# Optimization experiments

Measured on AMD Instinct MI355X. Metric: run time of the kernel, lower is better.

Reference implementation:

```python
import jax, jax.numpy as jnp
import numpy as np

N_NODES = 100000


def sage_conv(x, src, dst, W_l, W_r, b):
    """PyG-style SAGEConv with mean aggregation:
    out = mean_{j in N(i)} x_j @ W_l + b + x_i @ W_r
    Messages flow edge_index[0] (src) -> edge_index[1] (dst).
    """
    n = x.shape[0]
    msgs = x[src]  # [E, F] gather
    agg = jax.ops.segment_sum(msgs, dst, num_segments=n)  # [N, F]
    cnt = jax.ops.segment_sum(jnp.ones((src.shape[0],), dtype=x.dtype), dst, num_segments=n)
    mean = agg / jnp.clip(cnt, 1.0)[:, None]
    return mean @ W_l + b + x @ W_r


def setup_inputs() -> dict:
    key = jax.random.key(0)
    ks = jax.random.split(key, 12)
    F_in, H, out_c = 128, 128, 1
    E, K = 3200000, 64

    def glorot(k, shape):
        fan_in, fan_out = shape[0], shape[1]
        lim = np.sqrt(6.0 / (fan_in + fan_out))
        return jax.random.uniform(k, shape, jnp.float32, -lim, lim)

    return {
        "x": jax.random.normal(ks[0], (N_NODES, F_in), jnp.float32),
        "edge_index": jax.random.randint(ks[1], (2, E), 0, N_NODES, jnp.int64),
        "curr_idx": 123,
        "dest_idx": 4567,
        "neighbor_indices": jax.random.randint(ks[2], (K,), 0, N_NODES, jnp.int64),
        # conv1 params
        "W1_l": glorot(ks[3], (F_in, H)),
        "W1_r": glorot(ks[4], (F_in, H)),
        "b1": jnp.zeros((H,), jnp.float32),
        # conv2 params
        "W2_l": glorot(ks[5], (H, H)),
        "W2_r": glorot(ks[6], (H, H)),
        "b2": jnp.zeros((H,), jnp.float32),
        # MLP head
        "Wlin1": glorot(ks[7], (3 * H, H)),
        "blin1": jnp.zeros((H,), jnp.float32),
        "Wlin2": glorot(ks[8], (H, out_c)),
        "blin2": jnp.zeros((out_c,), jnp.float32),
    }


def reference(x, edge_index, curr_idx, dest_idx, neighbor_indices,
              W1_l, W1_r, b1, W2_l, W2_r, b2, Wlin1, blin1, Wlin2, blin2):
    src, dst = edge_index[0], edge_index[1]
    h = jax.nn.relu(sage_conv(x, src, dst, W1_l, W1_r, b1))
    node_embs = sage_conv(h, src, dst, W2_l, W2_r, b2)  # [N, H]

    curr_emb = node_embs[curr_idx]  # [H]
    dest_emb = node_embs[dest_idx]  # [H]
    nbr_embs = node_embs[neighbor_indices]  # [K, H]
    K = nbr_embs.shape[0]
    # batched version of the per-neighbor concat + 2-layer MLP
    cat = jnp.concatenate([
        jnp.broadcast_to(curr_emb, (K, curr_emb.shape[0])),
        jnp.broadcast_to(dest_emb, (K, dest_emb.shape[0])),
        nbr_embs,
    ], axis=1)  # [K, 3H]
    hidden = jax.nn.relu(cat @ Wlin1 + blin1)  # [K, H]
    q_values = hidden @ Wlin2 + blin2  # [K, 1]
    return q_values
```

## Files before the change

### kernel.cpp

```cpp
#include <hip/hip_runtime.h>
#include <cstdint>

constexpr int F        = 128;
constexpr int U_CAP    = 8192;
constexpr int T_CAP    = 128;
constexpr int E2_CAP   = 131072;
constexpr int BKT      = 128;
constexpr int BM_WORDS = 3200;
constexpr int SBLK     = 256;
constexpr int EPT      = 64;
constexpr int EPBLK    = SBLK * EPT;
constexpr int LCAP     = 512;


__global__ void k_zero(int* p, int n) {
    int i = blockIdx.x * blockDim.x + threadIdx.x;
    int stride = gridDim.x * blockDim.x;
    for (; i < n; i += stride) p[i] = 0;
}

__global__ void k_build(const int* eidx, int E, int N,
                        const int* curr, const int* dest, const int* nbr, int K,
                        int* hdr, int* t_map, int* u_map,
                        unsigned* t_bm, unsigned* u_bm,
                        int* t_node, int* ent2comp, int* ulist) {
    __shared__ int s_e64, s_n64;
    int tid = threadIdx.x;
    if (tid == 0) { s_e64 = 1; s_n64 = 1; }
    __syncthreads();
    if (tid < 64 && eidx[2 * tid + 1] != 0) s_e64 = 0;
    if (tid < K / 2 && nbr[2 * tid + 1] != 0) s_n64 = 0;
    __syncthreads();
    int n64 = s_n64;
    if (tid == 0) { hdr[4] = s_e64; hdr[5] = s_n64; }

    int node = -1;
    if (tid < K + 2) {
        if (tid == 0)      node = curr[0];
        else if (tid == 1) node = dest[0];
        else               node = n64 ? nbr[2 * (tid - 2)] : nbr[tid - 2];
        if ((unsigned)node < (unsigned)N) {
            if (atomicCAS(&t_map[node], 0, -1) == 0) {
                int slot = atomicAdd(&hdr[0], 1);
                t_node[slot] = node;
                int uid = atomicAdd(&hdr[1], 1);
                ulist[uid] = node;
                atomicExch(&u_map[node], uid + 1);
                if (node < BM_WORDS * 32) {
                    atomicOr(&t_bm[node >> 5], 1u << (node & 31));
                    atomicOr(&u_bm[node >> 5], 1u << (node & 31));
                }
                atomicExch(&t_map[node], slot + 1);
            }
        }
    }
    __syncthreads();
    if (tid < K + 2) {
        int v = ((unsigned)node < (unsigned)N) ? atomicAdd(&t_map[node], 0) : 1;
        ent2comp[tid] = v - 1;
    }
}

static __device__ __forceinline__ int esrc(const int* eidx, int E, int e, int is64) {
    return is64 ? eidx[2 * (size_t)e] : eidx[e];
}
static __device__ __forceinline__ int edst(const int* eidx, int E, int e, int is64) {
    return is64 ? eidx[2 * ((size_t)E + e)] : eidx[(size_t)E + e];
}

__global__ void k_scan1(const int* __restrict__ eidx, int E, int N,
                        const int* __restrict__ t_map, int* u_map,
                        const unsigned* __restrict__ t_bm, unsigned* u_bm,
                        int* hdr, int2* edges2, int* ulist) {
    __shared__ int l_cnt, l_base;
    __shared__ int2 l_buf[LCAP];
    int tid = threadIdx.x;
    if (tid == 0) l_cnt = 0;
    __syncthreads();
    int is64 = hdr[4];
    int be = blockIdx.x * EPBLK;
    int dv[EPT];
    #pragma unroll
    for (int r = 0; r < EPT / 4; ++r) {
        int e0 = be + (r * SBLK + tid) * 4;
        if (!is64 && e0 + 3 < E) {
            int4 d4 = *reinterpret_cast<const int4*>(eidx + (size_t)E + e0);
            dv[r*4+0] = d4.x; dv[r*4+1] = d4.y; dv[r*4+2] = d4.z; dv[r*4+3] = d4.w;
        } else {
            for (int q = 0; q < 4; ++q)
                dv[r*4+q] = (e0 + q < E) ? edst(eidx, E, e0 + q, is64) : -1;
        }
    }
    unsigned long long m = 0;
    #pragma unroll
    for (int i = 0; i < EPT; ++i) {
        int d  = dv[i];
        int dc = ((unsigned)d < (unsigned)N) ? d : 0;
        unsigned w = t_bm[dc >> 5];
        if ((unsigned)d < (unsigned)N && ((w >> (d & 31)) & 1))
            m |= (1ull << i);
    }
    while (m) {
        int i = __ffsll(m) - 1; m &= m - 1;
        int d = dv[i];
        int tm = t_map[d];
        if (tm <= 0) continue;
        int r = i >> 2, q = i & 3;
        int e = be + (r * SBLK + tid) * 4 + q;
        int s = esrc(eidx, E, e, is64);
        if ((unsigned)s >= (unsigned)N) continue;
        int p = atomicAdd(&l_cnt, 1);
        if (p < LCAP) l_buf[p] = make_int2(s, tm - 1);
        else {
            int gp = atomicAdd(&hdr[2], 1);
            if (gp < E2_CAP) edges2[gp] = make_int2(s, tm - 1);
        }
        if (atomicCAS(&u_map[s], 0, -1) == 0) {
            int id = atomicAdd(&hdr[1], 1);
            if (id < U_CAP) ulist[id] = s;
            if (s < BM_WORDS * 32) atomicOr(&u_bm[s >> 5], 1u << (s & 31));
            __threadfence();
            atomicExch(&u_map[s], id + 1);
        }
    }
    __syncthreads();
    int c = min(l_cnt, LCAP);
    if (c > 0) {
        if (tid == 0) l_base = atomicAdd(&hdr[2], c);
        __syncthreads();
        for (int i = tid; i < c; i += SBLK) {
            int gp = l_base + i;
            if (gp < E2_CAP) edges2[gp] = l_buf[i];
        }
    }
}

__global__ void k_scanU(const int* __restrict__ eidx, int E, int N,
                        const int* __restrict__ u_map,
                        const unsigned* __restrict__ u_bm,
                        const int* __restrict__ hdr,
                        int* deg1, int* bucket) {
    int tid = threadIdx.x;
    int is64 = hdr[4];
    int be = blockIdx.x * EPBLK;
    int dv[EPT];
    #pragma unroll
    for (int r = 0; r < EPT / 4; ++r) {
        int e0 = be + (r * SBLK + tid) * 4;
        if (!is64 && e0 + 3 < E) {
            int4 d4 = *reinterpret_cast<const int4*>(eidx + (size_t)E + e0);
            dv[r*4+0] = d4.x; dv[r*4+1] = d4.y; dv[r*4+2] = d4.z; dv[r*4+3] = d4.w;
        } else {
            for (int q = 0; q < 4; ++q)
                dv[r*4+q] = (e0 + q < E) ? edst(eidx, E, e0 + q, is64) : -1;
        }
    }
    unsigned long long m = 0;
    #pragma unroll
    for (int i = 0; i < EPT; ++i) {
        int d  = dv[i];
        int dc = ((unsigned)d < (unsigned)N) ? d : 0;
        unsigned w = u_bm[dc >> 5];
        if ((unsigned)d < (unsigned)N && ((w >> (d & 31)) & 1))
            m |= (1ull << i);
    }
    while (m) {
        int i = __ffsll(m) - 1; m &= m - 1;
        int d = dv[i];
        int um = u_map[d];
        if (um <= 0 || um > U_CAP) continue;
        int r = i >> 2, q = i & 3;
        int e = be + (r * SBLK + tid) * 4 + q;
        int s = esrc(eidx, E, e, is64);
        if ((unsigned)s >= (unsigned)N) continue;
        int slot = um - 1;
        int pos = atomicAdd(&deg1[slot], 1);
        if (pos < BKT) bucket[(size_t)slot * BKT + pos] = s;
    }
}

__global__ void k_l1(const int* __restrict__ deg1, const int* __restrict__ bucket,
                     const int* __restrict__ hdr, const int* __restrict__ ulist, int N,
                     const float* __restrict__ x,
                     const float* __restrict__ W1l, const float* __restrict__ W1r,
                     const float* __restrict__ b1, float* __restrict__ h) {
    int nU = min(hdr[1], U_CAP);
    __shared__ int s_src[BKT];
    __shared__ float4 s_part[4][32];
    __shared__ float mean[F];
    __shared__ float xr[F];
    int j = threadIdx.x;
    int g = j >> 5, l = j & 31;
    for (int b = blockIdx.x; b < nU; b += gridDim.x) {
        int dg = deg1[b];
        int stored = min(dg, BKT);
        if (j < stored) s_src[j] = bucket[(size_t)b * BKT + j];
        int node = ulist[b];
        xr[j] = ((unsigned)node < (unsigned)N) ? x[(size_t)node * F + j] : 0.0f;
        __syncthreads();
        float4 a4 = make_float4(0.f, 0.f, 0.f, 0.f);
        #pragma unroll 4
        for (int i = g; i < stored; i += 4) {
            int s = s_src[i];
            if ((unsigned)s < (unsigned)N) {
                float4 v = reinterpret_cast<const float4*>(x + (size_t)s * F)[l];
                a4.x += v.x; a4.y += v.y; a4.z += v.z; a4.w += v.w;
            }
        }
        s_part[g][l] = a4;
        __syncthreads();
        float c = (dg < 1) ? 1.0f : (float)dg;
        int lp = j >> 2, cc = j & 3;
        float sum = 0.0f;
        #pragma unroll
        for (int gg = 0; gg < 4; ++gg) {
            float4 p = s_part[gg][lp];
            sum += (cc == 0) ? p.x : (cc == 1) ? p.y : (cc == 2) ? p.z : p.w;
        }
        mean[j] = sum / c;
        __syncthreads();
        float o = b1[j];
        #pragma unroll 4
        for (int k = 0; k < F; ++k) {
            o += mean[k] * W1l[k * F + j];
            o += xr[k]   * W1r[k * F + j];
        }
        h[(size_t)b * F + j] = (o > 0.0f) ? o : 0.0f;
        __syncthreads();
    }
}

__global__ void k_l2(const int* __restrict__ hdr, const int* __restrict__ t_node,
                     const int* __restrict__ u_map, int N,
                     const int2* __restrict__ edges2, const float* __restrict__ h,
                     const float* __restrict__ W2l, const float* __restrict__ W2r,
                     const float* __restrict__ b2, float* __restrict__ embT) {
    int nT = min(hdr[0], T_CAP);
    int b  = blockIdx.x;
    if (b >= nT) return;
    int nE2 = min(hdr[2], E2_CAP);
    __shared__ int s_ui[256];
    __shared__ int s_cnt;
    __shared__ float mean[F];
    __shared__ float hr[F];
    int j = threadIdx.x;
    if (j == 0) s_cnt = 0;
    __syncthreads();
    for (int i = j; i < nE2; i += 128) {
        int2 ed = edges2[i];
        if (ed.y == b) {
            int ui = ((unsigned)ed.x < (unsigned)N) ? (u_map[ed.x] - 1) : -1;
            if ((unsigned)ui < (unsigned)U_CAP) {
                int p = atomicAdd(&s_cnt, 1);
                if (p < 256) s_ui[p] = ui;
            }
        }
    }
    __syncthreads();
    int cnt = min(s_cnt, 256);
    float sum = 0.0f;
    #pragma unroll 4
    for (int i = 0; i < cnt; ++i) sum += h[(size_t)s_ui[i] * F + j];
    float c = (s_cnt < 1) ? 1.0f : (float)s_cnt;
    mean[j] = sum / c;
    int node = t_node[b];
    int ui = ((unsigned)node < (unsigned)N) ? (u_map[node] - 1) : -1;
    hr[j] = ((unsigned)ui < (unsigned)U_CAP) ? h[(size_t)ui * F + j] : 0.0f;
    __syncthreads();
    float acc = b2[j];
    #pragma unroll 4
    for (int k = 0; k < F; ++k) {
        acc += mean[k] * W2l[k * F + j];
        acc += hr[k]   * W2r[k * F + j];
    }
    embT[(size_t)b * F + j] = acc;
}

static __device__ __forceinline__ float clamp999(int v) {
    return (float)(v < 0 ? 0 : (v > 999 ? 999 : v));
}

__global__ void k_headf(const int* __restrict__ hdr, const int* __restrict__ ent2comp,
                        const float* __restrict__ embT,
                        const float* __restrict__ Wlin1, const float* __restrict__ blin1,
                        const float* __restrict__ Wlin2, const float* __restrict__ blin2,
                        float* __restrict__ out, int K) {
    __shared__ float s_cat[3 * F];
    __shared__ float s_part[4][F];
    __shared__ float red[F];
    int k = blockIdx.x;
    int tid = threadIdx.x;
    int g = tid >> 7, j = tid & (F - 1);
    int c0 = ent2comp[0] & (T_CAP - 1);
    int c1 = ent2comp[1] & (T_CAP - 1);
    int ck = ent2comp[2 + k] & (T_CAP - 1);
    if (tid < F)          s_cat[tid] = embT[(size_t)c0 * F + tid];
    else if (tid < 2 * F) s_cat[tid] = embT[(size_t)c1 * F + (tid - F)];
    else if (tid < 3 * F) s_cat[tid] = embT[(size_t)ck * F + (tid - 2 * F)];
    __syncthreads();
    float acc = 0.0f;
    #pragma unroll 4
    for (int i = g * 96; i < (g + 1) * 96; ++i)
        acc += s_cat[i] * Wlin1[i * F + j];
    s_part[g][j] = acc;
    __syncthreads();
    if (g == 0) {
        float hid = blin1[j] + s_part[0][j] + s_part[1][j] + s_part[2][j] + s_part[3][j];
        hid = (hid > 0.0f) ? hid : 0.0f;
        red[j] = hid * Wlin2[j];
    }
    __syncthreads();
    for (int s = 64; s > 0; s >>= 1) {
        if (tid < s) red[tid] += red[tid + s];
        __syncthreads();
    }
    if (tid == 0) {
        int nT = hdr[0], nU = hdr[1], nE2 = hdr[2];
        float D = 0.0f;
        if      (nT  < 1  || nT  > K + 2)  D = 1.0e6f + clamp999(nT) * 1e3f;
        else if (nU  < nT || nU  > U_CAP)  D = 2.0e6f + clamp999(nU / 10) * 1e3f;
        else if (nE2 < 1  || nE2 > E2_CAP) D = 3.0e6f + clamp999(nE2 / 10) * 1e3f;
        out[k] = red[0] + blin2[0] + D;
    }
}

extern "C" void kernel_launch(void* const* d_in, const int* in_sizes, int n_in,
                              void* d_out, int out_size, void* d_ws, size_t ws_size,
                              hipStream_t stream) {
    const float* x     = (const float*)d_in[0];
    const int*   eidx  = (const int*)d_in[1];
    const int*   curr  = (const int*)d_in[2];
    const int*   dest  = (const int*)d_in[3];
    const int*   nbr   = (const int*)d_in[4];
    const float* W1l   = (const float*)d_in[5];
    const float* W1r   = (const float*)d_in[6];
    const float* b1    = (const float*)d_in[7];
    const float* W2l   = (const float*)d_in[8];
    const float* W2r   = (const float*)d_in[9];
    const float* b2    = (const float*)d_in[10];
    const float* Wlin1 = (const float*)d_in[11];
    const float* blin1 = (const float*)d_in[12];
    const float* Wlin2 = (const float*)d_in[13];
    const float* blin2 = (const float*)d_in[14];
    float* out = (float*)d_out;

    const int N = in_sizes[0] / F;
    const int E = in_sizes[1] / 2;
    const int K = in_sizes[4];

    char*  ws  = (char*)d_ws;
    size_t off = 0;
    int*      hdr      = (int*)(ws + off);      off += 64;
    int*      t_map    = (int*)(ws + off);      off += (size_t)4 * N;
    int*      u_map    = (int*)(ws + off);      off += (size_t)4 * N;
    int*      t_node   = (int*)(ws + off);      off += (size_t)4 * T_CAP;
    int*      ent2comp = (int*)(ws + off);      off += (size_t)4 * 256;
    int*      ulist    = (int*)(ws + off);      off += (size_t)4 * U_CAP;
    unsigned* t_bm     = (unsigned*)(ws + off); off += (size_t)4 * BM_WORDS;
    unsigned* u_bm     = (unsigned*)(ws + off); off += (size_t)4 * BM_WORDS;
    int*      deg1     = (int*)(ws + off);      off += (size_t)4 * U_CAP;
    size_t zero_bytes = off;
    int*      bucket   = (int*)(ws + off);      off += (size_t)4 * U_CAP * BKT;
    int2*     edges2   = (int2*)(ws + off);     off += (size_t)8 * E2_CAP;
    float*    h        = (float*)(ws + off);    off += (size_t)4 * U_CAP * F;
    float*    embT     = (float*)(ws + off);    off += (size_t)4 * T_CAP * F;

    int zero_words = (int)(zero_bytes / 4);
    k_zero<<<1024, 256, 0, stream>>>((int*)d_ws, zero_words);

    k_build<<<1, 128, 0, stream>>>(eidx, E, N, curr, dest, nbr, K, hdr, t_map, u_map,
                                   t_bm, u_bm, t_node, ent2comp, ulist);

    int sg = (E + EPBLK - 1) / EPBLK;
    k_scan1<<<sg, SBLK, 0, stream>>>(eidx, E, N, t_map, u_map, t_bm, u_bm,
                                     hdr, edges2, ulist);
    k_scanU<<<sg, SBLK, 0, stream>>>(eidx, E, N, u_map, u_bm, hdr, deg1, bucket);
    k_l1<<<2048, 128, 0, stream>>>(deg1, bucket, hdr, ulist, N, x, W1l, W1r, b1, h);
    k_l2<<<T_CAP, 128, 0, stream>>>(hdr, t_node, u_map, N, edges2, h, W2l, W2r, b2, embT);
    k_headf<<<K, 512, 0, stream>>>(hdr, ent2comp, embT, Wlin1, blin1, Wlin2, blin2, out, K);
}
```

Baseline: 255.8 us.

## Reuse scanU buckets for layer-2 aggregation and vectorize int64 edge scans

The separate target-edge list built in the first scan is removed. Layer 2 now reads each target's in-neighbours from the per-node buckets that the second scan already fills, so the first scan only has to discover the 1-hop source set. Both scans process edges inline through a probe lambda instead of buffering 64 destinations per thread in registers. They read int64 edge indices with int4 vector loads, and edges per thread drop from 64 to 16. The cost is that layer 2 relies on bucket truncation at BKT, and the edge-list count check disappears from the diagnostics.

```diff
diff --git a/kernel.cpp b/kernel.cpp
--- a/kernel.cpp
+++ b/kernel.cpp
@@ -4,13 +4,11 @@
 constexpr int F        = 128;
 constexpr int U_CAP    = 8192;
 constexpr int T_CAP    = 128;
-constexpr int E2_CAP   = 131072;
 constexpr int BKT      = 128;
 constexpr int BM_WORDS = 3200;
 constexpr int SBLK     = 256;
-constexpr int EPT      = 64;
+constexpr int EPT      = 16;
 constexpr int EPBLK    = SBLK * EPT;
-constexpr int LCAP     = 512;
 
 
 __global__ void k_zero(int* p, int n) {
@@ -61,60 +59,20 @@
     }
 }
 
-static __device__ __forceinline__ int esrc(const int* eidx, int E, int e, int is64) {
-    return is64 ? eidx[2 * (size_t)e] : eidx[e];
-}
-static __device__ __forceinline__ int edst(const int* eidx, int E, int e, int is64) {
-    return is64 ? eidx[2 * ((size_t)E + e)] : eidx[(size_t)E + e];
-}
-
 __global__ void k_scan1(const int* __restrict__ eidx, int E, int N,
-                        const int* __restrict__ t_map, int* u_map,
-                        const unsigned* __restrict__ t_bm, unsigned* u_bm,
-                        int* hdr, int2* edges2, int* ulist) {
-    __shared__ int l_cnt, l_base;
-    __shared__ int2 l_buf[LCAP];
+                        int* __restrict__ u_map,
+                        const unsigned* __restrict__ t_bm,
+                        unsigned* __restrict__ u_bm,
+                        int* __restrict__ hdr, int* __restrict__ ulist) {
     int tid = threadIdx.x;
-    if (tid == 0) l_cnt = 0;
-    __syncthreads();
     int is64 = hdr[4];
-    int be = blockIdx.x * EPBLK;
-    int dv[EPT];
-    #pragma unroll
-    for (int r = 0; r < EPT / 4; ++r) {
-        int e0 = be + (r * SBLK + tid) * 4;
-        if (!is64 && e0 + 3 < E) {
-            int4 d4 = *reinterpret_cast<const int4*>(eidx + (size_t)E + e0);
-            dv[r*4+0] = d4.x; dv[r*4+1] = d4.y; dv[r*4+2] = d4.z; dv[r*4+3] = d4.w;
-        } else {
-            for (int q = 0; q < 4; ++q)
-                dv[r*4+q] = (e0 + q < E) ? edst(eidx, E, e0 + q, is64) : -1;
-        }
-    }
-    unsigned long long m = 0;
-    #pragma unroll
-    for (int i = 0; i < EPT; ++i) {
-        int d  = dv[i];
-        int dc = ((unsigned)d < (unsigned)N) ? d : 0;
-        unsigned w = t_bm[dc >> 5];
-        if ((unsigned)d < (unsigned)N && ((w >> (d & 31)) & 1))
-            m |= (1ull << i);
-    }
-    while (m) {
-        int i = __ffsll(m) - 1; m &= m - 1;
-        int d = dv[i];
-        int tm = t_map[d];
-        if (tm <= 0) continue;
-        int r = i >> 2, q = i & 3;
-        int e = be + (r * SBLK + tid) * 4 + q;
-        int s = esrc(eidx, E, e, is64);
-        if ((unsigned)s >= (unsigned)N) continue;
-        int p = atomicAdd(&l_cnt, 1);
-        if (p < LCAP) l_buf[p] = make_int2(s, tm - 1);
-        else {
-            int gp = atomicAdd(&hdr[2], 1);
-            if (gp < E2_CAP) edges2[gp] = make_int2(s, tm - 1);
-        }
+    size_t be = (size_t)blockIdx.x * EPBLK;
+
+    auto probe = [&](int d, size_t e) {
+        if ((unsigned)d >= (unsigned)N) return;
+        if (!((t_bm[d >> 5] >> (d & 31)) & 1)) return;
+        int s = is64 ? eidx[2 * e] : eidx[e];
+        if ((unsigned)s >= (unsigned)N) return;
         if (atomicCAS(&u_map[s], 0, -1) == 0) {
             int id = atomicAdd(&hdr[1], 1);
             if (id < U_CAP) ulist[id] = s;
@@ -122,15 +80,41 @@
             __threadfence();
             atomicExch(&u_map[s], id + 1);
         }
-    }
-    __syncthreads();
-    int c = min(l_cnt, LCAP);
-    if (c > 0) {
-        if (tid == 0) l_base = atomicAdd(&hdr[2], c);
-        __syncthreads();
-        for (int i = tid; i < c; i += SBLK) {
-            int gp = l_base + i;
-            if (gp < E2_CAP) edges2[gp] = l_buf[i];
+    };
+
+    if (is64) {
+        if (((E & 1) == 0) && be + EPBLK <= (size_t)E) {
+            #pragma unroll
+            for (int r = 0; r < EPT / 2; ++r) {
+                size_t e0 = be + (size_t)(r * SBLK + tid) * 2;
+                int4 v = *reinterpret_cast<const int4*>(eidx + 2 * ((size_t)E + e0));
+                probe(v.x, e0);
+                probe(v.z, e0 + 1);
+            }
+        } else {
+            #pragma unroll
+            for (int r = 0; r < EPT / 2; ++r) {
+                size_t e0 = be + (size_t)(r * SBLK + tid) * 2;
+                if (e0 < (size_t)E)     probe(eidx[2 * ((size_t)E + e0)],     e0);
+                if (e0 + 1 < (size_t)E) probe(eidx[2 * ((size_t)E + e0 + 1)], e0 + 1);
+            }
+        }
+    } else {
+        if (((E & 3) == 0) && be + EPBLK <= (size_t)E) {
+            #pragma unroll
+            for (int r = 0; r < EPT / 4; ++r) {
+                size_t e0 = be + (size_t)(r * SBLK + tid) * 4;
+                int4 v = *reinterpret_cast<const int4*>(eidx + (size_t)E + e0);
+                probe(v.x, e0); probe(v.y, e0 + 1); probe(v.z, e0 + 2); probe(v.w, e0 + 3);
+            }
+        } else {
+            #pragma unroll
+            for (int r = 0; r < EPT / 4; ++r) {
+                size_t e0 = be + (size_t)(r * SBLK + tid) * 4;
+                #pragma unroll
+                for (int q = 0; q < 4; ++q)
+                    if (e0 + q < (size_t)E) probe(eidx[(size_t)E + e0 + q], e0 + q);
+            }
         }
     }
 }
@@ -139,43 +123,57 @@
                         const int* __restrict__ u_map,
                         const unsigned* __restrict__ u_bm,
                         const int* __restrict__ hdr,
-                        int* deg1, int* bucket) {
+                        int* __restrict__ deg1, int* __restrict__ bucket) {
     int tid = threadIdx.x;
     int is64 = hdr[4];
-    int be = blockIdx.x * EPBLK;
-    int dv[EPT];
-    #pragma unroll
-    for (int r = 0; r < EPT / 4; ++r) {
-        int e0 = be + (r * SBLK + tid) * 4;
-        if (!is64 && e0 + 3 < E) {
-            int4 d4 = *reinterpret_cast<const int4*>(eidx + (size_t)E + e0);
-            dv[r*4+0] = d4.x; dv[r*4+1] = d4.y; dv[r*4+2] = d4.z; dv[r*4+3] = d4.w;
-        } else {
-            for (int q = 0; q < 4; ++q)
-                dv[r*4+q] = (e0 + q < E) ? edst(eidx, E, e0 + q, is64) : -1;
-        }
-    }
-    unsigned long long m = 0;
-    #pragma unroll
-    for (int i = 0; i < EPT; ++i) {
-        int d  = dv[i];
-        int dc = ((unsigned)d < (unsigned)N) ? d : 0;
-        unsigned w = u_bm[dc >> 5];
-        if ((unsigned)d < (unsigned)N && ((w >> (d & 31)) & 1))
-            m |= (1ull << i);
-    }
-    while (m) {
-        int i = __ffsll(m) - 1; m &= m - 1;
-        int d = dv[i];
+    size_t be = (size_t)blockIdx.x * EPBLK;
+
+    auto probe = [&](int d, size_t e) {
+        if ((unsigned)d >= (unsigned)N) return;
+        if (!((u_bm[d >> 5] >> (d & 31)) & 1)) return;
         int um = u_map[d];
-        if (um <= 0 || um > U_CAP) continue;
-        int r = i >> 2, q = i & 3;
-        int e = be + (r * SBLK + tid) * 4 + q;
-        int s = esrc(eidx, E, e, is64);
-        if ((unsigned)s >= (unsigned)N) continue;
+        if (um <= 0 || um > U_CAP) return;
+        int s = is64 ? eidx[2 * e] : eidx[e];
+        if ((unsigned)s >= (unsigned)N) return;
         int slot = um - 1;
         int pos = atomicAdd(&deg1[slot], 1);
         if (pos < BKT) bucket[(size_t)slot * BKT + pos] = s;
+    };
+
+    if (is64) {
+        if (((E & 1) == 0) && be + EPBLK <= (size_t)E) {
+            #pragma unroll
+            for (int r = 0; r < EPT / 2; ++r) {
+                size_t e0 = be + (size_t)(r * SBLK + tid) * 2;
+                int4 v = *reinterpret_cast<const int4*>(eidx + 2 * ((size_t)E + e0));
+                probe(v.x, e0);
+                probe(v.z, e0 + 1);
+            }
+        } else {
+            #pragma unroll
+            for (int r = 0; r < EPT / 2; ++r) {
+                size_t e0 = be + (size_t)(r * SBLK + tid) * 2;
+                if (e0 < (size_t)E)     probe(eidx[2 * ((size_t)E + e0)],     e0);
+                if (e0 + 1 < (size_t)E) probe(eidx[2 * ((size_t)E + e0 + 1)], e0 + 1);
+            }
+        }
+    } else {
+        if (((E & 3) == 0) && be + EPBLK <= (size_t)E) {
+            #pragma unroll
+            for (int r = 0; r < EPT / 4; ++r) {
+                size_t e0 = be + (size_t)(r * SBLK + tid) * 4;
+                int4 v = *reinterpret_cast<const int4*>(eidx + (size_t)E + e0);
+                probe(v.x, e0); probe(v.y, e0 + 1); probe(v.z, e0 + 2); probe(v.w, e0 + 3);
+            }
+        } else {
+            #pragma unroll
+            for (int r = 0; r < EPT / 4; ++r) {
+                size_t e0 = be + (size_t)(r * SBLK + tid) * 4;
+                #pragma unroll
+                for (int q = 0; q < 4; ++q)
+                    if (e0 + q < (size_t)E) probe(eidx[(size_t)E + e0 + q], e0 + q);
+            }
+        }
     }
 }
 
@@ -232,40 +230,39 @@
 
 __global__ void k_l2(const int* __restrict__ hdr, const int* __restrict__ t_node,
                      const int* __restrict__ u_map, int N,
-                     const int2* __restrict__ edges2, const float* __restrict__ h,
+                     const int* __restrict__ deg1, const int* __restrict__ bucket,
+                     const float* __restrict__ h,
                      const float* __restrict__ W2l, const float* __restrict__ W2r,
                      const float* __restrict__ b2, float* __restrict__ embT) {
     int nT = min(hdr[0], T_CAP);
     int b  = blockIdx.x;
     if (b >= nT) return;
-    int nE2 = min(hdr[2], E2_CAP);
-    __shared__ int s_ui[256];
-    __shared__ int s_cnt;
+    __shared__ int s_ui[BKT];
     __shared__ float mean[F];
     __shared__ float hr[F];
     int j = threadIdx.x;
-    if (j == 0) s_cnt = 0;
-    __syncthreads();
-    for (int i = j; i < nE2; i += 128) {
-        int2 ed = edges2[i];
-        if (ed.y == b) {
-            int ui = ((unsigned)ed.x < (unsigned)N) ? (u_map[ed.x] - 1) : -1;
-            if ((unsigned)ui < (unsigned)U_CAP) {
-                int p = atomicAdd(&s_cnt, 1);
-                if (p < 256) s_ui[p] = ui;
-            }
-        }
-    }
-    __syncthreads();
-    int cnt = min(s_cnt, 256);
+    int node = t_node[b];
+    int tui = ((unsigned)node < (unsigned)N) ? (u_map[node] - 1) : -1;
+    int dg = 0, stored = 0;
+    if ((unsigned)tui < (unsigned)U_CAP) {
+        dg = deg1[tui];
+        stored = min(dg, BKT);
+    }
+    if (j < stored) {
+        int s  = bucket[(size_t)tui * BKT + j];
+        int ui = ((unsigned)s < (unsigned)N) ? (u_map[s] - 1) : -1;
+        s_ui[j] = ((unsigned)ui < (unsigned)U_CAP) ? ui : -1;
+    }
+    hr[j] = ((unsigned)tui < (unsigned)U_CAP) ? h[(size_t)tui * F + j] : 0.0f;
+    __syncthreads();
     float sum = 0.0f;
     #pragma unroll 4
-    for (int i = 0; i < cnt; ++i) sum += h[(size_t)s_ui[i] * F + j];
-    float c = (s_cnt < 1) ? 1.0f : (float)s_cnt;
+    for (int i = 0; i < stored; ++i) {
+        int ui = s_ui[i];
+        if (ui >= 0) sum += h[(size_t)ui * F + j];
+    }
+    float c = (dg < 1) ? 1.0f : (float)dg;
     mean[j] = sum / c;
-    int node = t_node[b];
-    int ui = ((unsigned)node < (unsigned)N) ? (u_map[node] - 1) : -1;
-    hr[j] = ((unsigned)ui < (unsigned)U_CAP) ? h[(size_t)ui * F + j] : 0.0f;
     __syncthreads();
     float acc = b2[j];
     #pragma unroll 4
@@ -315,11 +312,10 @@
         __syncthreads();
     }
     if (tid == 0) {
-        int nT = hdr[0], nU = hdr[1], nE2 = hdr[2];
+        int nT = hdr[0], nU = hdr[1];
         float D = 0.0f;
-        if      (nT  < 1  || nT  > K + 2)  D = 1.0e6f + clamp999(nT) * 1e3f;
-        else if (nU  < nT || nU  > U_CAP)  D = 2.0e6f + clamp999(nU / 10) * 1e3f;
-        else if (nE2 < 1  || nE2 > E2_CAP) D = 3.0e6f + clamp999(nE2 / 10) * 1e3f;
+        if      (nT < 1  || nT > K + 2)  D = 1.0e6f + clamp999(nT) * 1e3f;
+        else if (nU < nT || nU > U_CAP)  D = 2.0e6f + clamp999(nU / 10) * 1e3f;
         out[k] = red[0] + blin2[0] + D;
     }
 }
@@ -361,7 +357,6 @@
     int*      deg1     = (int*)(ws + off);      off += (size_t)4 * U_CAP;
     size_t zero_bytes = off;
     int*      bucket   = (int*)(ws + off);      off += (size_t)4 * U_CAP * BKT;
-    int2*     edges2   = (int2*)(ws + off);     off += (size_t)8 * E2_CAP;
     float*    h        = (float*)(ws + off);    off += (size_t)4 * U_CAP * F;
     float*    embT     = (float*)(ws + off);    off += (size_t)4 * T_CAP * F;
 
@@ -372,10 +367,10 @@
                                    t_bm, u_bm, t_node, ent2comp, ulist);
 
     int sg = (E + EPBLK - 1) / EPBLK;
-    k_scan1<<<sg, SBLK, 0, stream>>>(eidx, E, N, t_map, u_map, t_bm, u_bm,
-                                     hdr, edges2, ulist);
+    k_scan1<<<sg, SBLK, 0, stream>>>(eidx, E, N, u_map, t_bm, u_bm, hdr, ulist);
     k_scanU<<<sg, SBLK, 0, stream>>>(eidx, E, N, u_map, u_bm, hdr, deg1, bucket);
     k_l1<<<2048, 128, 0, stream>>>(deg1, bucket, hdr, ulist, N, x, W1l, W1r, b1, h);
-    k_l2<<<T_CAP, 128, 0, stream>>>(hdr, t_node, u_map, N, edges2, h, W2l, W2r, b2, embT);
+    k_l2<<<T_CAP, 128, 0, stream>>>(hdr, t_node, u_map, N, deg1, bucket, h,
+                                    W2l, W2r, b2, embT);
     k_headf<<<K, 512, 0, stream>>>(hdr, ent2comp, embT, Wlin1, blin1, Wlin2, blin2, out, K);
 }
```

Result: no change. 258.6 us (+1.1%).
